# Performance work log

Measured on AMD Instinct MI355X. Metric: run time of the kernel, lower is better.

Reference implementation:

```python
import jax, jax.numpy as jnp
import numpy as np

B, L, D = 4, 4096, 1024
NEG_BIG = -1e30  # finite stand-in for log(0) to keep vjp NaN-free; exp underflows to 0


def log_g(x):
    # log of g(x) = where(x>=0, x+0.5, sigmoid(x)); log-space, branch-safe
    return jnp.where(x >= 0.0, jnp.log(jax.nn.relu(x) + 0.5), -jax.nn.softplus(-x))


def setup_inputs() -> dict:
    key = jax.random.key(0)
    ks = jax.random.split(key, 4)
    std = np.sqrt(2.0 / D)  # kaiming_normal for fan_in = D
    x = jax.random.normal(ks[0], (B, L, D), dtype=jnp.float32)
    W_f = jax.random.normal(ks[1], (D, D), dtype=jnp.float32) * std
    W_i = jax.random.normal(ks[2], (D, D), dtype=jnp.float32) * std
    W_h = jax.random.normal(ks[3], (D, D), dtype=jnp.float32) * std
    b_f = jnp.zeros((D,), dtype=jnp.float32)
    b_i = jnp.zeros((D,), dtype=jnp.float32)
    b_h = jnp.zeros((D,), dtype=jnp.float32)
    return {"x": x, "W_f": W_f, "b_f": b_f, "W_i": W_i, "b_i": b_i, "W_h": W_h, "b_h": b_h}


def reference(x, W_f, b_f, W_i, b_i, W_h, b_h):
    # gate pre-activations: (B, L, D)
    f_pre = jnp.einsum('bld,ed->ble', x, W_f) + b_f
    i_pre = jnp.einsum('bld,ed->ble', x, W_i) + b_i
    h_pre = jnp.einsum('bld,ed->ble', x, W_h) + b_h

    # log-space normalized gates: log_f + log_i parametrize f/(f+i), i/(f+i)
    diff = jax.nn.softplus(-f_pre) - jax.nn.softplus(-i_pre)
    log_f = -jax.nn.softplus(diff)
    log_i = -jax.nn.softplus(-diff)
    log_tilde_h = log_g(h_pre)

    b, l, d = x.shape
    log_h0 = jnp.full((b, 1, d), NEG_BIG, dtype=x.dtype)  # log(0)
    log_values = jnp.concatenate([log_h0, log_i + log_tilde_h], axis=1)  # (B, L+1, D)

    # associative parallel scan in log space
    a_star = jnp.pad(jnp.cumsum(log_f, axis=1), ((0, 0), (1, 0), (0, 0)))  # (B, L+1, D)
    log_h = a_star + jax.lax.cumlogsumexp(log_values - a_star, axis=1)
    return jnp.exp(log_h)[:, 1:]  # (B, L, D)
```

## Files before the change

### kernel.cpp

```cpp
#include <hip/hip_runtime.h>

#define M_TOTAL 16384
#define N_DIM   1024
#define K_DIM   1024
#define L_SEQ   4096
#define B_SZ    4
#define D_DIM   1024
#define CH      64
#define NCHUNK  (L_SEQ / CH)
#define NCHAN   (B_SZ * D_DIM)

#define BM 128
#define BN 128
#define BK 64
#define NKT (K_DIM / BK)
#define TPB 512

typedef __attribute__((ext_vector_type(8))) short v8s;
typedef __attribute__((ext_vector_type(4))) float f32x4;

#define SB0()   __builtin_amdgcn_sched_barrier(0)
#define BAR()   __builtin_amdgcn_s_barrier()
#define WAITL0() do { asm volatile("s_waitcnt lgkmcnt(0)" ::: "memory"); SB0(); } while (0)
#define WAITL4() do { asm volatile("s_waitcnt lgkmcnt(4)" ::: "memory"); SB0(); } while (0)
#define WAITV0() do { asm volatile("s_waitcnt vmcnt(0)"   ::: "memory"); SB0(); } while (0)
#define AS1 __attribute__((address_space(1)))
#define AS3 __attribute__((address_space(3)))

__device__ __forceinline__ ushort f2b(float f) {
  uint u = __float_as_uint(f);
  u += 0x7FFFu + ((u >> 16) & 1u);
  return (ushort)(u >> 16);
}
__device__ __forceinline__ float b2f(ushort u) {
  return __uint_as_float(((uint)u) << 16);
}

__global__ void cast_f32_bf16(const float* __restrict__ src, ushort* __restrict__ dst, int n4) {
  int i = blockIdx.x * blockDim.x + threadIdx.x;
  if (i >= n4) return;
  float4 v = reinterpret_cast<const float4*>(src)[i];
  ushort4 o = make_ushort4(f2b(v.x), f2b(v.y), f2b(v.z), f2b(v.w));
  reinterpret_cast<ushort4*>(dst)[i] = o;
}

__global__ void cast_w3(const float* __restrict__ s0, const float* __restrict__ s1,
                        const float* __restrict__ s2,
                        ushort* __restrict__ o0, ushort* __restrict__ o1, ushort* __restrict__ o2) {
  int i = blockIdx.x * blockDim.x + threadIdx.x;
  const float* s = (blockIdx.y == 0) ? s0 : (blockIdx.y == 1) ? s1 : s2;
  ushort* o      = (blockIdx.y == 0) ? o0 : (blockIdx.y == 1) ? o1 : o2;
  float4 v = reinterpret_cast<const float4*>(s)[i];
  ushort4 t = make_ushort4(f2b(v.x), f2b(v.y), f2b(v.z), f2b(v.w));
  reinterpret_cast<ushort4*>(o)[i] = t;
}

__device__ __forceinline__ void gates(float fp, float ip, float hp, float& a, float& v) {
  float Ef = __expf(-fp);
  float Ei = __expf(-ip);
  float r  = __builtin_amdgcn_rcpf(2.f + Ef + Ei);
  float f  = (1.f + Ei) * r;
  float i  = (1.f + Ef) * r;
  float ht = (hp >= 0.f) ? (hp + 0.5f) : __builtin_amdgcn_rcpf(1.f + __expf(-hp));
  a = f;
  v = i * ht;
}

__launch_bounds__(TPB, 2)
__global__ void gemm_fused(const ushort* __restrict__ X,
                           const ushort* __restrict__ W0, const ushort* __restrict__ W1,
                           const ushort* __restrict__ W2,
                           const float* __restrict__ bfp, const float* __restrict__ bip,
                           const float* __restrict__ bhp,
                           uint* __restrict__ Pav)
{
  __shared__ ushort lds[2][4][BM * BK];

  const int id  = blockIdx.x;
  const int x_  = id & 7;
  const int k_  = id >> 3;
  const int sub = k_ >> 6;
  const int l2_ = k_ & 63;
  const int n0 = (l2_ & 7) * BN;
  const int m0 = (x_ * 16 + sub * 8 + (l2_ >> 3)) * BM;

  const int tid  = threadIdx.x;
  const int lane = tid & 63;
  const int w    = tid >> 6;
  const int wr   = w >> 2;
  const int wc   = w & 3;
  const int fr   = lane & 15, g = lane >> 4;

  int aoffh[4][2], boffh[2][2];
#pragma unroll
  for (int q = 0; q < 4; ++q)
#pragma unroll
    for (int ks = 0; ks < 2; ++ks) {
      int row = wr * 64 + q * 16 + fr;
      aoffh[q][ks] = row * BK + (((ks * 4 + g) ^ (row & 7)) << 3);
    }
#pragma unroll
  for (int n = 0; n < 2; ++n)
#pragma unroll
    for (int ks = 0; ks < 2; ++ks) {
      int row = wc * 32 + n * 16 + fr;
      boffh[n][ks] = row * BK + (((ks * 4 + g) ^ (row & 7)) << 3);
    }

  const int s0 = tid, s1 = 512 + tid;
  const int r0 = s0 >> 3, k0 = (s0 & 7) ^ (r0 & 7);
  const int r1 = s1 >> 3, k1 = (s1 & 7) ^ (r1 & 7);
  const int d0 = s0 * 8, d1 = s1 * 8;

  const ushort* gsrc[4][2];
  gsrc[0][0] = X  + (size_t)(m0 + r0) * K_DIM + k0 * 8;
  gsrc[0][1] = X  + (size_t)(m0 + r1) * K_DIM + k1 * 8;
  gsrc[1][0] = W0 + (size_t)(n0 + r0) * K_DIM + k0 * 8;
  gsrc[1][1] = W0 + (size_t)(n0 + r1) * K_DIM + k1 * 8;
  gsrc[2][0] = W1 + (size_t)(n0 + r0) * K_DIM + k0 * 8;
  gsrc[2][1] = W1 + (size_t)(n0 + r1) * K_DIM + k1 * 8;
  gsrc[3][0] = W2 + (size_t)(n0 + r0) * K_DIM + k0 * 8;
  gsrc[3][1] = W2 + (size_t)(n0 + r1) * K_DIM + k1 * 8;

  auto issue = [&](int buf, int mat, int kt, int j) {
    const ushort* s_ = gsrc[mat][j] + kt * BK;
    __builtin_amdgcn_global_load_lds((const AS1 void*)s_,
        (AS3 void*)(&lds[buf][mat][j ? d1 : d0]), 16, 0, 0);
  };

  f32x4 acc[3][4][2] = {};

#pragma unroll
  for (int mat = 0; mat < 4; ++mat) { issue(0, mat, 0, 0); issue(0, mat, 0, 1); }
  WAITV0();
  BAR(); SB0();

  int cur = 0;
  for (int t = 0; t < NKT; ++t) {
    const bool pf = (t + 1 < NKT);
    const ushort* rb = &lds[cur][0][0];
    v8s aF[4][2], bA[2][2], bB[2][2];

#pragma unroll
    for (int q = 0; q < 4; ++q)
#pragma unroll
      for (int ks = 0; ks < 2; ++ks)
        aF[q][ks] = *reinterpret_cast<const v8s*>(rb + aoffh[q][ks]);
#pragma unroll
    for (int n = 0; n < 2; ++n)
#pragma unroll
      for (int ks = 0; ks < 2; ++ks)
        bA[n][ks] = *reinterpret_cast<const v8s*>(rb + 1 * BM * BK + boffh[n][ks]);
    SB0();
    if (pf) {
#pragma unroll
      for (int mat = 0; mat < 4; ++mat) { issue(cur ^ 1, mat, t + 1, 0); issue(cur ^ 1, mat, t + 1, 1); }
    }
    SB0();
#pragma unroll
    for (int n = 0; n < 2; ++n)
#pragma unroll
      for (int ks = 0; ks < 2; ++ks)
        bB[n][ks] = *reinterpret_cast<const v8s*>(rb + 2 * BM * BK + boffh[n][ks]);
    SB0();
    WAITL4();
    __builtin_amdgcn_s_setprio(1);
#pragma unroll
    for (int ks = 0; ks < 2; ++ks)
#pragma unroll
      for (int mi = 0; mi < 4; ++mi) {
        acc[0][mi][0] = __builtin_amdgcn_mfma_f32_16x16x32_bf16(aF[mi][ks], bA[0][ks], acc[0][mi][0], 0, 0, 0);
        acc[0][mi][1] = __builtin_amdgcn_mfma_f32_16x16x32_bf16(aF[mi][ks], bA[1][ks], acc[0][mi][1], 0, 0, 0);
      }
    __builtin_amdgcn_s_setprio(0);
#pragma unroll
    for (int n = 0; n < 2; ++n)
#pragma unroll
      for (int ks = 0; ks < 2; ++ks)
        bA[n][ks] = *reinterpret_cast<const v8s*>(rb + 3 * BM * BK + boffh[n][ks]);
    SB0();
    WAITL4();
    __builtin_amdgcn_s_setprio(1);
#pragma unroll
    for (int ks = 0; ks < 2; ++ks)
#pragma unroll
      for (int mi = 0; mi < 4; ++mi) {
        acc[1][mi][0] = __builtin_amdgcn_mfma_f32_16x16x32_bf16(aF[mi][ks], bB[0][ks], acc[1][mi][0], 0, 0, 0);
        acc[1][mi][1] = __builtin_amdgcn_mfma_f32_16x16x32_bf16(aF[mi][ks], bB[1][ks], acc[1][mi][1], 0, 0, 0);
      }
    __builtin_amdgcn_s_setprio(0);
    WAITL0();
    __builtin_amdgcn_s_setprio(1);
#pragma unroll
    for (int ks = 0; ks < 2; ++ks)
#pragma unroll
      for (int mi = 0; mi < 4; ++mi) {
        acc[2][mi][0] = __builtin_amdgcn_mfma_f32_16x16x32_bf16(aF[mi][ks], bA[0][ks], acc[2][mi][0], 0, 0, 0);
        acc[2][mi][1] = __builtin_amdgcn_mfma_f32_16x16x32_bf16(aF[mi][ks], bA[1][ks], acc[2][mi][1], 0, 0, 0);
      }
    __builtin_amdgcn_s_setprio(0);

    if (pf) {
      WAITV0();
      BAR(); SB0();
      cur ^= 1;
    }
  }

#pragma unroll
  for (int ni = 0; ni < 2; ++ni) {
    const int col = n0 + wc * 32 + ni * 16 + fr;
    const float vbf = bfp[col], vbi = bip[col], vbh = bhp[col];
#pragma unroll
    for (int mi = 0; mi < 4; ++mi) {
      const int row0 = m0 + wr * 64 + mi * 16 + g * 4;
#pragma unroll
      for (int r = 0; r < 4; ++r) {
        float a, v;
        gates(acc[0][mi][ni][r] + vbf, acc[1][mi][ni][r] + vbi, acc[2][mi][ni][r] + vbh, a, v);
        Pav[(size_t)(row0 + r) * N_DIM + col] = (uint)f2b(a) | ((uint)f2b(v) << 16);
      }
    }
  }
}

__global__ void scan_pass1(const uint4* __restrict__ Pav4,
                           float4* __restrict__ AggA, float4* __restrict__ AggV)
{
  int tid = blockIdx.x * blockDim.x + threadIdx.x;
  int c4 = tid & 1023;
  int chunk = tid >> 10;
  int b = c4 >> 8;
  int d4 = c4 & 255;
  size_t base4 = ((size_t)b * L_SEQ + (size_t)chunk * CH) * (D_DIM / 4) + d4;
  float A0 = 1.f, A1 = 1.f, A2 = 1.f, A3 = 1.f;
  float V0 = 0.f, V1 = 0.f, V2 = 0.f, V3 = 0.f;
#pragma unroll 4
  for (int t = 0; t < CH; ++t) {
    uint4 u = Pav4[base4 + (size_t)t * (D_DIM / 4)];
    float a0 = b2f((ushort)(u.x & 0xFFFFu)), v0 = b2f((ushort)(u.x >> 16));
    float a1 = b2f((ushort)(u.y & 0xFFFFu)), v1 = b2f((ushort)(u.y >> 16));
    float a2 = b2f((ushort)(u.z & 0xFFFFu)), v2 = b2f((ushort)(u.z >> 16));
    float a3 = b2f((ushort)(u.w & 0xFFFFu)), v3 = b2f((ushort)(u.w >> 16));
    A0 *= a0; V0 = fmaf(a0, V0, v0);
    A1 *= a1; V1 = fmaf(a1, V1, v1);
    A2 *= a2; V2 = fmaf(a2, V2, v2);
    A3 *= a3; V3 = fmaf(a3, V3, v3);
  }
  AggA[(size_t)chunk * (NCHAN / 4) + c4] = make_float4(A0, A1, A2, A3);
  AggV[(size_t)chunk * (NCHAN / 4) + c4] = make_float4(V0, V1, V2, V3);
}

__global__ void scan_mid(const float4* __restrict__ AggA, const float4* __restrict__ AggV,
                         float4* __restrict__ Start)
{
  int c4 = blockIdx.x * blockDim.x + threadIdx.x;
  float4 h = make_float4(0.f, 0.f, 0.f, 0.f);
#pragma unroll
  for (int j = 0; j < NCHUNK; ++j) {
    float4 A = AggA[(size_t)j * (NCHAN / 4) + c4];
    float4 V = AggV[(size_t)j * (NCHAN / 4) + c4];
    Start[(size_t)j * (NCHAN / 4) + c4] = h;
    h.x = fmaf(A.x, h.x, V.x);
    h.y = fmaf(A.y, h.y, V.y);
    h.z = fmaf(A.z, h.z, V.z);
    h.w = fmaf(A.w, h.w, V.w);
  }
}

__global__ void scan_pass2(const uint4* __restrict__ Pav4,
                           const float4* __restrict__ Start, float4* __restrict__ out4)
{
  int tid = blockIdx.x * blockDim.x + threadIdx.x;
  int c4 = tid & 1023;
  int chunk = tid >> 10;
  int b = c4 >> 8;
  int d4 = c4 & 255;
  size_t base4 = ((size_t)b * L_SEQ + (size_t)chunk * CH) * (D_DIM / 4) + d4;
  float4 h = Start[(size_t)chunk * (NCHAN / 4) + c4];
#pragma unroll 4
  for (int t = 0; t < CH; ++t) {
    size_t idx = base4 + (size_t)t * (D_DIM / 4);
    uint4 u = Pav4[idx];
    h.x = fmaf(b2f((ushort)(u.x & 0xFFFFu)), h.x, b2f((ushort)(u.x >> 16)));
    h.y = fmaf(b2f((ushort)(u.y & 0xFFFFu)), h.y, b2f((ushort)(u.y >> 16)));
    h.z = fmaf(b2f((ushort)(u.z & 0xFFFFu)), h.z, b2f((ushort)(u.z >> 16)));
    h.w = fmaf(b2f((ushort)(u.w & 0xFFFFu)), h.w, b2f((ushort)(u.w >> 16)));
    out4[idx] = h;
  }
}

extern "C" void kernel_launch(void* const* d_in, const int* in_sizes, int n_in,
                              void* d_out, int out_size, void* d_ws, size_t ws_size,
                              hipStream_t stream) {
  (void)in_sizes; (void)n_in; (void)out_size; (void)ws_size;
  const float* x  = (const float*)d_in[0];
  const float* Wf = (const float*)d_in[1];
  const float* bf = (const float*)d_in[2];
  const float* Wi = (const float*)d_in[3];
  const float* bi = (const float*)d_in[4];
  const float* Wh = (const float*)d_in[5];
  const float* bh = (const float*)d_in[6];

  ushort* xb  = (ushort*)d_ws;
  ushort* wfb = xb  + (size_t)M_TOTAL * K_DIM;
  ushort* wib = wfb + (size_t)N_DIM * K_DIM;
  ushort* whb = wib + (size_t)N_DIM * K_DIM;
  uint*  Pav  = (uint*)(whb + (size_t)N_DIM * K_DIM);
  float* AggA  = (float*)(Pav + (size_t)M_TOTAL * N_DIM);
  float* AggV  = AggA + NCHAN * NCHUNK;
  float* Start = AggV + NCHAN * NCHUNK;

  cast_f32_bf16<<<(M_TOTAL * K_DIM / 4) / 256, 256, 0, stream>>>(x, xb, M_TOTAL * K_DIM / 4);
  cast_w3<<<dim3((N_DIM * K_DIM / 4) / 256, 3), 256, 0, stream>>>(Wf, Wi, Wh, wfb, wib, whb);

  gemm_fused<<<dim3((M_TOTAL / BM) * (N_DIM / BN)), TPB, 0, stream>>>(
      xb, wfb, wib, whb, bf, bi, bh, Pav);

  scan_pass1<<<(NCHAN / 4 * NCHUNK) / 256, 256, 0, stream>>>(
      (const uint4*)Pav, (float4*)AggA, (float4*)AggV);
  scan_mid<<<(NCHAN / 4) / 256, 256, 0, stream>>>(
      (const float4*)AggA, (const float4*)AggV, (float4*)Start);
  scan_pass2<<<(NCHAN / 4 * NCHUNK) / 256, 256, 0, stream>>>(
      (const uint4*)Pav, (const float4*)Start, (float4*)d_out);
}
```

Before: 176.4 us.

## Switch fused gate GEMM to 32x32x16 MFMA tiles and simplify block swizzle

Replaces the 16x16x32 bf16 MFMA fragments with 32x32x16 instructions, so each wave computes two 32x32 output tiles per gate matrix. This changes the LDS fragment offsets, accumulator layout and epilogue row mapping. The larger MFMA shape halves the B-fragment LDS reads per wave and reduces the instruction count for the same work. The block-index swizzle is also changed to a simpler mapping, which alters L2 reuse of X and W tiles across concurrently running blocks.

```diff
diff --git a/kernel.cpp b/kernel.cpp
--- a/kernel.cpp
+++ b/kernel.cpp
@@ -16,8 +16,8 @@
 #define NKT (K_DIM / BK)
 #define TPB 512
 
-typedef __attribute__((ext_vector_type(8))) short v8s;
-typedef __attribute__((ext_vector_type(4))) float f32x4;
+typedef __attribute__((ext_vector_type(8)))  short v8s;
+typedef __attribute__((ext_vector_type(16))) float f32x16;
 
 #define SB0()   __builtin_amdgcn_sched_barrier(0)
 #define BAR()   __builtin_amdgcn_s_barrier()
@@ -77,35 +77,31 @@
   __shared__ ushort lds[2][4][BM * BK];
 
   const int id  = blockIdx.x;
-  const int x_  = id & 7;
-  const int k_  = id >> 3;
-  const int sub = k_ >> 6;
-  const int l2_ = k_ & 63;
-  const int n0 = (l2_ & 7) * BN;
-  const int m0 = (x_ * 16 + sub * 8 + (l2_ >> 3)) * BM;
+  const int sw  = (id & 7) * 128 + (id >> 3);
+  const int n0  = (sw & 7) * BN;
+  const int m0  = (sw >> 3) * BM;
 
   const int tid  = threadIdx.x;
   const int lane = tid & 63;
   const int w    = tid >> 6;
   const int wr   = w >> 2;
   const int wc   = w & 3;
-  const int fr   = lane & 15, g = lane >> 4;
-
-  int aoffh[4][2], boffh[2][2];
-#pragma unroll
-  for (int q = 0; q < 4; ++q)
-#pragma unroll
-    for (int ks = 0; ks < 2; ++ks) {
-      int row = wr * 64 + q * 16 + fr;
-      aoffh[q][ks] = row * BK + (((ks * 4 + g) ^ (row & 7)) << 3);
+  const int lo   = lane & 31;
+  const int hi   = lane >> 5;
+
+  int aoffh[2][4], boffh[4];
+#pragma unroll
+  for (int m = 0; m < 2; ++m)
+#pragma unroll
+    for (int ks = 0; ks < 4; ++ks) {
+      int row = wr * 64 + m * 32 + lo;
+      aoffh[m][ks] = row * BK + (((ks * 2 + hi) ^ (row & 7)) << 3);
     }
 #pragma unroll
-  for (int n = 0; n < 2; ++n)
-#pragma unroll
-    for (int ks = 0; ks < 2; ++ks) {
-      int row = wc * 32 + n * 16 + fr;
-      boffh[n][ks] = row * BK + (((ks * 4 + g) ^ (row & 7)) << 3);
-    }
+  for (int ks = 0; ks < 4; ++ks) {
+    int row = wc * 32 + lo;
+    boffh[ks] = row * BK + (((ks * 2 + hi) ^ (row & 7)) << 3);
+  }
 
   const int s0 = tid, s1 = 512 + tid;
   const int r0 = s0 >> 3, k0 = (s0 & 7) ^ (r0 & 7);
@@ -128,7 +124,7 @@
         (AS3 void*)(&lds[buf][mat][j ? d1 : d0]), 16, 0, 0);
   };
 
-  f32x4 acc[3][4][2] = {};
+  f32x16 acc[3][2] = {};
 
 #pragma unroll
   for (int mat = 0; mat < 4; ++mat) { issue(0, mat, 0, 0); issue(0, mat, 0, 1); }
@@ -139,18 +135,16 @@
   for (int t = 0; t < NKT; ++t) {
     const bool pf = (t + 1 < NKT);
     const ushort* rb = &lds[cur][0][0];
-    v8s aF[4][2], bA[2][2], bB[2][2];
-
-#pragma unroll
-    for (int q = 0; q < 4; ++q)
-#pragma unroll
-      for (int ks = 0; ks < 2; ++ks)
-        aF[q][ks] = *reinterpret_cast<const v8s*>(rb + aoffh[q][ks]);
-#pragma unroll
-    for (int n = 0; n < 2; ++n)
-#pragma unroll
-      for (int ks = 0; ks < 2; ++ks)
-        bA[n][ks] = *reinterpret_cast<const v8s*>(rb + 1 * BM * BK + boffh[n][ks]);
+    v8s aF[2][4], b0[4], b1[4], b2[4];
+
+#pragma unroll
+    for (int m = 0; m < 2; ++m)
+#pragma unroll
+      for (int ks = 0; ks < 4; ++ks)
+        aF[m][ks] = *reinterpret_cast<const v8s*>(rb + aoffh[m][ks]);
+#pragma unroll
+    for (int ks = 0; ks < 4; ++ks)
+      b0[ks] = *reinterpret_cast<const v8s*>(rb + 1 * BM * BK + boffh[ks]);
     SB0();
     if (pf) {
 #pragma unroll
@@ -158,46 +152,36 @@
     }
     SB0();
 #pragma unroll
-    for (int n = 0; n < 2; ++n)
-#pragma unroll
-      for (int ks = 0; ks < 2; ++ks)
-        bB[n][ks] = *reinterpret_cast<const v8s*>(rb + 2 * BM * BK + boffh[n][ks]);
+    for (int ks = 0; ks < 4; ++ks)
+      b1[ks] = *reinterpret_cast<const v8s*>(rb + 2 * BM * BK + boffh[ks]);
     SB0();
     WAITL4();
     __builtin_amdgcn_s_setprio(1);
 #pragma unroll
-    for (int ks = 0; ks < 2; ++ks)
-#pragma unroll
-      for (int mi = 0; mi < 4; ++mi) {
-        acc[0][mi][0] = __builtin_amdgcn_mfma_f32_16x16x32_bf16(aF[mi][ks], bA[0][ks], acc[0][mi][0], 0, 0, 0);
-        acc[0][mi][1] = __builtin_amdgcn_mfma_f32_16x16x32_bf16(aF[mi][ks], bA[1][ks], acc[0][mi][1], 0, 0, 0);
-      }
+    for (int ks = 0; ks < 4; ++ks)
+#pragma unroll
+      for (int m = 0; m < 2; ++m)
+        acc[0][m] = __builtin_amdgcn_mfma_f32_32x32x16_bf16(aF[m][ks], b0[ks], acc[0][m], 0, 0, 0);
     __builtin_amdgcn_s_setprio(0);
 #pragma unroll
-    for (int n = 0; n < 2; ++n)
-#pragma unroll
-      for (int ks = 0; ks < 2; ++ks)
-        bA[n][ks] = *reinterpret_cast<const v8s*>(rb + 3 * BM * BK + boffh[n][ks]);
+    for (int ks = 0; ks < 4; ++ks)
+      b2[ks] = *reinterpret_cast<const v8s*>(rb + 3 * BM * BK + boffh[ks]);
     SB0();
     WAITL4();
     __builtin_amdgcn_s_setprio(1);
 #pragma unroll
-    for (int ks = 0; ks < 2; ++ks)
-#pragma unroll
-      for (int mi = 0; mi < 4; ++mi) {
-        acc[1][mi][0] = __builtin_amdgcn_mfma_f32_16x16x32_bf16(aF[mi][ks], bB[0][ks], acc[1][mi][0], 0, 0, 0);
-        acc[1][mi][1] = __builtin_amdgcn_mfma_f32_16x16x32_bf16(aF[mi][ks], bB[1][ks], acc[1][mi][1], 0, 0, 0);
-      }
+    for (int ks = 0; ks < 4; ++ks)
+#pragma unroll
+      for (int m = 0; m < 2; ++m)
+        acc[1][m] = __builtin_amdgcn_mfma_f32_32x32x16_bf16(aF[m][ks], b1[ks], acc[1][m], 0, 0, 0);
     __builtin_amdgcn_s_setprio(0);
     WAITL0();
     __builtin_amdgcn_s_setprio(1);
 #pragma unroll
-    for (int ks = 0; ks < 2; ++ks)
-#pragma unroll
-      for (int mi = 0; mi < 4; ++mi) {
-        acc[2][mi][0] = __builtin_amdgcn_mfma_f32_16x16x32_bf16(aF[mi][ks], bA[0][ks], acc[2][mi][0], 0, 0, 0);
-        acc[2][mi][1] = __builtin_amdgcn_mfma_f32_16x16x32_bf16(aF[mi][ks], bA[1][ks], acc[2][mi][1], 0, 0, 0);
-      }
+    for (int ks = 0; ks < 4; ++ks)
+#pragma unroll
+      for (int m = 0; m < 2; ++m)
+        acc[2][m] = __builtin_amdgcn_mfma_f32_32x32x16_bf16(aF[m][ks], b2[ks], acc[2][m], 0, 0, 0);
     __builtin_amdgcn_s_setprio(0);
 
     if (pf) {
@@ -207,19 +191,17 @@
     }
   }
 
-#pragma unroll
-  for (int ni = 0; ni < 2; ++ni) {
-    const int col = n0 + wc * 32 + ni * 16 + fr;
-    const float vbf = bfp[col], vbi = bip[col], vbh = bhp[col];
-#pragma unroll
-    for (int mi = 0; mi < 4; ++mi) {
-      const int row0 = m0 + wr * 64 + mi * 16 + g * 4;
-#pragma unroll
-      for (int r = 0; r < 4; ++r) {
-        float a, v;
-        gates(acc[0][mi][ni][r] + vbf, acc[1][mi][ni][r] + vbi, acc[2][mi][ni][r] + vbh, a, v);
-        Pav[(size_t)(row0 + r) * N_DIM + col] = (uint)f2b(a) | ((uint)f2b(v) << 16);
-      }
+  const int col = n0 + wc * 32 + lo;
+  const float vbf = bfp[col], vbi = bip[col], vbh = bhp[col];
+#pragma unroll
+  for (int m = 0; m < 2; ++m) {
+    const int rbase = m0 + wr * 64 + m * 32 + 4 * hi;
+#pragma unroll
+    for (int r = 0; r < 16; ++r) {
+      const int row = rbase + (r & 3) + 8 * (r >> 2);
+      float a, v;
+      gates(acc[0][m][r] + vbf, acc[1][m][r] + vbi, acc[2][m][r] + vbh, a, v);
+      Pav[(size_t)row * N_DIM + col] = (uint)f2b(a) | ((uint)f2b(v) << 16);
     }
   }
 }
```

New measurement: 194.6 us. +10.4%, slower.

## Fuse chunk-aggregate scan pass into GEMM epilogue and simplify block swizzle

Applied to the files above, without the earlier changes.

The GEMM epilogue now computes each 64-row chunk's (product of a, affine v) aggregate in registers, using in-lane reduction plus wave shuffles, and writes AggA/AggV directly. This removes the separate scan_pass1 kernel, along with its full re-read of the packed gate tensor and one launch. Aggregates are now formed from fp32 gate values rather than the bf16-rounded ones that pass2 later reads, a small numeric mismatch. The block-to-tile mapping is also replaced with a simpler interleave, which changes L2 reuse patterns for X and W tiles.

```diff
diff --git a/kernel.cpp b/kernel.cpp
--- a/kernel.cpp
+++ b/kernel.cpp
@@ -72,17 +72,15 @@
                            const ushort* __restrict__ W2,
                            const float* __restrict__ bfp, const float* __restrict__ bip,
                            const float* __restrict__ bhp,
-                           uint* __restrict__ Pav)
+                           uint* __restrict__ Pav,
+                           float* __restrict__ AggA, float* __restrict__ AggV)
 {
   __shared__ ushort lds[2][4][BM * BK];
 
   const int id  = blockIdx.x;
-  const int x_  = id & 7;
-  const int k_  = id >> 3;
-  const int sub = k_ >> 6;
-  const int l2_ = k_ & 63;
-  const int n0 = (l2_ & 7) * BN;
-  const int m0 = (x_ * 16 + sub * 8 + (l2_ >> 3)) * BM;
+  const int sw  = (id & 7) * 128 + (id >> 3);
+  const int n0  = (sw & 7) * BN;
+  const int m0  = (sw >> 3) * BM;
 
   const int tid  = threadIdx.x;
   const int lane = tid & 63;
@@ -207,48 +205,43 @@
     }
   }
 
+  const int bidx = m0 >> 12;
+  const int jch  = ((m0 & 4095) >> 6) + wr;
 #pragma unroll
   for (int ni = 0; ni < 2; ++ni) {
     const int col = n0 + wc * 32 + ni * 16 + fr;
     const float vbf = bfp[col], vbi = bip[col], vbh = bhp[col];
+    float BAgg[4], VAgg[4];
 #pragma unroll
     for (int mi = 0; mi < 4; ++mi) {
       const int row0 = m0 + wr * 64 + mi * 16 + g * 4;
+      float RA = 1.f, RV = 0.f;
 #pragma unroll
       for (int r = 0; r < 4; ++r) {
         float a, v;
         gates(acc[0][mi][ni][r] + vbf, acc[1][mi][ni][r] + vbi, acc[2][mi][ni][r] + vbh, a, v);
         Pav[(size_t)(row0 + r) * N_DIM + col] = (uint)f2b(a) | ((uint)f2b(v) << 16);
-      }
+        RA *= a; RV = fmaf(a, RV, v);
+      }
+      {
+        float pA = __shfl_xor(RA, 16), pV = __shfl_xor(RV, 16);
+        if (((lane >> 4) & 1) == 0) { RV = fmaf(pA, RV, pV); RA = RA * pA; }
+        else                        { RV = fmaf(RA, pV, RV); RA = RA * pA; }
+        pA = __shfl_xor(RA, 32); pV = __shfl_xor(RV, 32);
+        if (((lane >> 5) & 1) == 0) { RV = fmaf(pA, RV, pV); RA = RA * pA; }
+        else                        { RV = fmaf(RA, pV, RV); RA = RA * pA; }
+      }
+      BAgg[mi] = RA; VAgg[mi] = RV;
+    }
+    float CA = BAgg[0], CV = VAgg[0];
+#pragma unroll
+    for (int mi = 1; mi < 4; ++mi) { CV = fmaf(BAgg[mi], CV, VAgg[mi]); CA *= BAgg[mi]; }
+    if (g == 0) {
+      const int c = bidx * D_DIM + col;
+      AggA[jch * NCHAN + c] = CA;
+      AggV[jch * NCHAN + c] = CV;
     }
   }
-}
-
-__global__ void scan_pass1(const uint4* __restrict__ Pav4,
-                           float4* __restrict__ AggA, float4* __restrict__ AggV)
-{
-  int tid = blockIdx.x * blockDim.x + threadIdx.x;
-  int c4 = tid & 1023;
-  int chunk = tid >> 10;
-  int b = c4 >> 8;
-  int d4 = c4 & 255;
-  size_t base4 = ((size_t)b * L_SEQ + (size_t)chunk * CH) * (D_DIM / 4) + d4;
-  float A0 = 1.f, A1 = 1.f, A2 = 1.f, A3 = 1.f;
-  float V0 = 0.f, V1 = 0.f, V2 = 0.f, V3 = 0.f;
-#pragma unroll 4
-  for (int t = 0; t < CH; ++t) {
-    uint4 u = Pav4[base4 + (size_t)t * (D_DIM / 4)];
-    float a0 = b2f((ushort)(u.x & 0xFFFFu)), v0 = b2f((ushort)(u.x >> 16));
-    float a1 = b2f((ushort)(u.y & 0xFFFFu)), v1 = b2f((ushort)(u.y >> 16));
-    float a2 = b2f((ushort)(u.z & 0xFFFFu)), v2 = b2f((ushort)(u.z >> 16));
-    float a3 = b2f((ushort)(u.w & 0xFFFFu)), v3 = b2f((ushort)(u.w >> 16));
-    A0 *= a0; V0 = fmaf(a0, V0, v0);
-    A1 *= a1; V1 = fmaf(a1, V1, v1);
-    A2 *= a2; V2 = fmaf(a2, V2, v2);
-    A3 *= a3; V3 = fmaf(a3, V3, v3);
-  }
-  AggA[(size_t)chunk * (NCHAN / 4) + c4] = make_float4(A0, A1, A2, A3);
-  AggV[(size_t)chunk * (NCHAN / 4) + c4] = make_float4(V0, V1, V2, V3);
 }
 
 __global__ void scan_mid(const float4* __restrict__ AggA, const float4* __restrict__ AggV,
@@ -315,10 +308,8 @@
   cast_w3<<<dim3((N_DIM * K_DIM / 4) / 256, 3), 256, 0, stream>>>(Wf, Wi, Wh, wfb, wib, whb);
 
   gemm_fused<<<dim3((M_TOTAL / BM) * (N_DIM / BN)), TPB, 0, stream>>>(
-      xb, wfb, wib, whb, bf, bi, bh, Pav);
-
-  scan_pass1<<<(NCHAN / 4 * NCHUNK) / 256, 256, 0, stream>>>(
-      (const uint4*)Pav, (float4*)AggA, (float4*)AggV);
+      xb, wfb, wib, whb, bf, bi, bh, Pav, AggA, AggV);
+
   scan_mid<<<(NCHAN / 4) / 256, 256, 0, stream>>>(
       (const float4*)AggA, (const float4*)AggV, (float4*)Start);
   scan_pass2<<<(NCHAN / 4 * NCHUNK) / 256, 256, 0, stream>>>(
```

Result: faster. 169.9 us (-3.7%).
